# Optimization experiments

Hardware: AMD Instinct MI355X
Metric: run time of the kernel (lower is better)

## Reference

```python
import jax, jax.numpy as jnp
import numpy as np

N_NODES = 50000
N_EDGES = 800000
DIM = 128


def setup_inputs() -> dict:
    key = jax.random.key(0)
    k_x, k_e, k_w1, k_w2 = jax.random.split(key, 4)
    x = jax.random.normal(k_x, (N_NODES, DIM), dtype=jnp.float32)
    edge_index = jax.random.randint(k_e, (2, N_EDGES), 0, N_NODES, dtype=jnp.int64)
    scale = 1.0 / np.sqrt(DIM)
    W1 = jax.random.normal(k_w1, (DIM, DIM), dtype=jnp.float32) * scale
    b1 = jnp.zeros((DIM,), dtype=jnp.float32)
    W2 = jax.random.normal(k_w2, (DIM, DIM), dtype=jnp.float32) * scale
    b2 = jnp.zeros((DIM,), dtype=jnp.float32)
    return {"x": x, "edge_index": edge_index, "W1": W1, "b1": b1, "W2": W2, "b2": b2}


def _gcn_conv(x, W, b, src, dst, n_nodes):
    """PyG GCNConv: D^{-1/2}(A+I)D^{-1/2} (x @ W) + b, self-loops added."""
    h = x @ W  # [N, D]
    ones = jnp.ones(src.shape[0], dtype=h.dtype)
    # degree of A+I, counting incoming edges at target nodes plus self-loop
    deg = jax.ops.segment_sum(ones, dst, num_segments=n_nodes) + 1.0
    dinv = jax.lax.rsqrt(deg)  # [N]
    norm = dinv[src] * dinv[dst]  # [E]
    msgs = h[src] * norm[:, None]  # [E, D] gather (memory-bound)
    agg = jax.ops.segment_sum(msgs, dst, num_segments=n_nodes)  # scatter-add
    agg = agg + h * (dinv * dinv)[:, None]  # self-loop contribution
    return agg + b


def reference(x, edge_index, W1, b1, W2, b2):
    src, dst = edge_index[0], edge_index[1]
    n = x.shape[0]
    identity = x
    out = jax.nn.relu(_gcn_conv(x, W1, b1, src, dst, n))
    out = _gcn_conv(out, W2, b2, src, dst, n)
    return jax.nn.relu(out + identity)
```

## Files before the change

kernel.cpp:

```cpp
#include <hip/hip_runtime.h>

#define N_NODES 50000
#define N_EDGES 800000
#define DIM 128
#define NB 391
#define CAP 2560
#define NCH 7
#define BIN_CHUNK 4096
#define BIN_BLOCKS 196
#define PREP_BLOCKS 64
#define GEMM_TILES 782
#define AGG_BLOCKS 3125

typedef unsigned int uint;
typedef unsigned short ushort;
typedef __attribute__((ext_vector_type(8))) __bf16 bf16x8;
typedef __attribute__((ext_vector_type(4))) float f32x4;

__device__ __forceinline__ uint f2bf(float f) {
    uint u = __float_as_uint(f);
    return (u + 0x7FFFu + ((u >> 16) & 1u)) >> 16;
}
__device__ __forceinline__ float2 bf2f2(uint u) {
    return make_float2(__uint_as_float(u << 16), __uint_as_float(u & 0xFFFF0000u));
}


__global__ __launch_bounds__(256) void binprep_kernel(const int* __restrict__ ei,
                                                      int* __restrict__ bincursor,
                                                      uint* __restrict__ pairs,
                                                      const float* __restrict__ W1,
                                                      const float* __restrict__ W2,
                                                      uint* __restrict__ Wt1,
                                                      uint* __restrict__ Wt2) {
    if (blockIdx.x >= BIN_BLOCKS) {
        int idx = (blockIdx.x - BIN_BLOCKS) * 256 + threadIdx.x;
        const float* W = (idx < 8192) ? W1 : W2;
        uint* Wt = (idx < 8192) ? Wt1 : Wt2;
        int i = idx & 8191;
        int n = i >> 6, k2 = i & 63;
        Wt[i] = f2bf(W[(2 * k2) * DIM + n]) | (f2bf(W[(2 * k2 + 1) * DIM + n]) << 16);
        return;
    }
    __shared__ int lh[NB];
    __shared__ int lbase[NB];
    int t = threadIdx.x;
    int eb = blockIdx.x * BIN_CHUNK;

    for (int b = t; b < NB; b += 256) lh[b] = 0;
    __syncthreads();

    int s_reg[16], d_reg[16];
#pragma unroll
    for (int i = 0; i < 16; ++i) {
        int e = eb + i * 256 + t;
        if (e < N_EDGES) {
            s_reg[i] = ei[e];
            d_reg[i] = ei[N_EDGES + e];
            atomicAdd(&lh[d_reg[i] >> 7], 1);
        } else {
            d_reg[i] = -1;
        }
    }
    __syncthreads();

    for (int b = t; b < NB; b += 256) {
        int c = lh[b];
        lbase[b] = c ? (b * CAP + atomicAdd(&bincursor[b], c)) : 0;
    }
    __syncthreads();
    for (int b = t; b < NB; b += 256) lh[b] = 0;
    __syncthreads();

#pragma unroll
    for (int i = 0; i < 16; ++i) {
        int d = d_reg[i];
        if (d >= 0) {
            int bin = d >> 7;
            int r = atomicAdd(&lh[bin], 1);
            pairs[lbase[bin] + r] = ((uint)s_reg[i] << 7) | (uint)(d & 127);
        }
    }
}


__device__ __forceinline__ void gemm1_tile(const float* __restrict__ X,
                                           const uint* __restrict__ Wt, int base,
                                           uint* __restrict__ Hout) {
    int t = threadIdx.x;
    int wv = t >> 6;
    int l = t & 63;
    int col = l & 15;
    int g = l >> 4;
    int grow = base + wv * 16 + col;
    int ar = grow > N_NODES - 1 ? N_NODES - 1 : grow;

    bf16x8 af[4];
    const float4* Xr = (const float4*)(X + (size_t)ar * DIM);
#pragma unroll
    for (int kk = 0; kk < 4; ++kk) {
        float4 x0 = Xr[kk * 8 + g * 2];
        float4 x1 = Xr[kk * 8 + g * 2 + 1];
        uint4 p;
        p.x = f2bf(x0.x) | (f2bf(x0.y) << 16);
        p.y = f2bf(x0.z) | (f2bf(x0.w) << 16);
        p.z = f2bf(x1.x) | (f2bf(x1.y) << 16);
        p.w = f2bf(x1.z) | (f2bf(x1.w) << 16);
        af[kk] = __builtin_bit_cast(bf16x8, p);
    }

    const uint4* Wr = (const uint4*)Wt;
    f32x4 acc[8];
#pragma unroll
    for (int n = 0; n < 8; ++n) acc[n] = (f32x4){0.f, 0.f, 0.f, 0.f};

#pragma unroll
    for (int n = 0; n < 8; ++n) {
        const uint4* wrow = Wr + (size_t)(n * 16 + col) * 16;
#pragma unroll
        for (int kk = 0; kk < 4; ++kk) {
            bf16x8 bf = __builtin_bit_cast(bf16x8, wrow[kk * 4 + g]);
            acc[n] = __builtin_amdgcn_mfma_f32_16x16x32_bf16(af[kk], bf, acc[n], 0, 0, 0);
        }
    }

#pragma unroll
    for (int j = 0; j < 4; ++j) {
        int row = base + wv * 16 + g * 4 + j;
        if (row < N_NODES) {
            ushort* hrow = (ushort*)(Hout + (size_t)row * 64);
#pragma unroll
            for (int n = 0; n < 8; ++n) hrow[n * 16 + col] = (ushort)f2bf(acc[n][j]);
        }
    }
}


__global__ __launch_bounds__(256) void fillgemm_kernel(const uint* __restrict__ pairs,
                                                       const int* __restrict__ bincursor,
                                                       int* __restrict__ rowbeg,
                                                       int* __restrict__ rowend,
                                                       float* __restrict__ dinv,
                                                       int* __restrict__ csr_src,
                                                       const float* __restrict__ x,
                                                       const uint* __restrict__ Wt1,
                                                       uint* __restrict__ Hs) {
    if (blockIdx.x >= NB) {
        gemm1_tile(x, Wt1, (blockIdx.x - NB) * 64, Hs);
        return;
    }
    __shared__ int cnt[128 * 8];
    __shared__ int nsum[128];
    __shared__ int nbase[128];
    int t = threadIdx.x;
    int blk = blockIdx.x;
    int bs = blk * CAP;
    int be = bs + bincursor[blk];

    for (int i = t; i < 128 * 8; i += 256) cnt[i] = 0;
    __syncthreads();

    for (int p = bs + t; p < be; p += 256) {
        uint pr = pairs[p];
        atomicAdd(&cnt[(pr & 127u) * 8 + (pr >> 20)], 1);
    }
    __syncthreads();

    if (t < 128) {
        int s = 0;
#pragma unroll
        for (int c = 0; c < NCH; ++c) s += cnt[t * 8 + c];
        nsum[t] = s;
        nbase[t] = s;
    }
    __syncthreads();
#pragma unroll
    for (int off = 1; off < 128; off <<= 1) {
        int v = (t < 128 && t >= off) ? nbase[t - off] : 0;
        __syncthreads();
        if (t < 128) nbase[t] += v;
        __syncthreads();
    }

    if (t < 128) {
        int deg = nsum[t];
        int ex = nbase[t] - deg;
        int node = blk * 128 + t;
        if (node < N_NODES) {
            rowbeg[node] = bs + ex;
            rowend[node] = bs + nbase[t];
            dinv[node] = rsqrtf((float)deg + 1.0f);
        }
        int run = ex;
#pragma unroll
        for (int c = 0; c < NCH; ++c) {
            int v = cnt[t * 8 + c];
            cnt[t * 8 + c] = run;
            run += v;
        }
    }
    __syncthreads();

    for (int p = bs + t; p < be; p += 256) {
        uint pr = pairs[p];
        int r = atomicAdd(&cnt[(pr & 127u) * 8 + (pr >> 20)], 1);
        csr_src[bs + r] = (int)(pr >> 7);
    }
}


template <bool DSRC, bool OBF>
__global__ __launch_bounds__(256) void agg_kernel(const int* __restrict__ rowbeg,
                                                  const int* __restrict__ rowend,
                                                  const int* __restrict__ csr_src,
                                                  const uint* __restrict__ Hs,
                                                  const float* __restrict__ dinv,
                                                  const float* __restrict__ bias,
                                                  const float* __restrict__ resid,
                                                  void* __restrict__ outv) {
    int gt = blockIdx.x * 256 + threadIdx.x;
    int wave = gt >> 6;
    int lane = gt & 63;
    int grp = lane >> 4;
    int li = lane & 15;
    int node = wave * 4 + grp;

    int beg = rowbeg[node];
    int end = rowend[node];
    float di = dinv[node];

    const uint4* H4 = (const uint4*)Hs;
    float a0, a1, a2, a3, a4, a5, a6, a7;
    {
        uint4 su = H4[(size_t)node * 16 + li];
        float2 v0 = bf2f2(su.x), v1 = bf2f2(su.y), v2 = bf2f2(su.z), v3 = bf2f2(su.w);
        float sf = DSRC ? di : 1.0f;
        a0 = sf * v0.x; a1 = sf * v0.y; a2 = sf * v1.x; a3 = sf * v1.y;
        a4 = sf * v2.x; a5 = sf * v2.y; a6 = sf * v3.x; a7 = sf * v3.y;
    }

#define ADDF8(u, f)                                                               \
    {                                                                             \
        float2 v0 = bf2f2(u.x), v1 = bf2f2(u.y), v2 = bf2f2(u.z), v3 = bf2f2(u.w);\
        a0 += f * v0.x; a1 += f * v0.y; a2 += f * v1.x; a3 += f * v1.y;           \
        a4 += f * v2.x; a5 += f * v2.y; a6 += f * v3.x; a7 += f * v3.y;           \
    }

    int e = beg;
    for (; e + 7 < end; e += 8) {
        int s[8];
#pragma unroll
        for (int i = 0; i < 8; ++i) s[i] = csr_src[e + i];
        uint4 u[8];
#pragma unroll
        for (int i = 0; i < 8; ++i) u[i] = H4[(size_t)s[i] * 16 + li];
        float f[8];
#pragma unroll
        for (int i = 0; i < 8; ++i) f[i] = DSRC ? dinv[s[i]] : 1.0f;
#pragma unroll
        for (int i = 0; i < 8; ++i) ADDF8(u[i], f[i]);
    }
    if (e + 3 < end) {
        int s[4];
#pragma unroll
        for (int i = 0; i < 4; ++i) s[i] = csr_src[e + i];
        uint4 u[4];
#pragma unroll
        for (int i = 0; i < 4; ++i) u[i] = H4[(size_t)s[i] * 16 + li];
        float f[4];
#pragma unroll
        for (int i = 0; i < 4; ++i) f[i] = DSRC ? dinv[s[i]] : 1.0f;
#pragma unroll
        for (int i = 0; i < 4; ++i) ADDF8(u[i], f[i]);
        e += 4;
    }
    for (; e < end; ++e) {
        int s = csr_src[e];
        uint4 u = H4[(size_t)s * 16 + li];
        float f = DSRC ? dinv[s] : 1.0f;
        ADDF8(u, f);
    }
#undef ADDF8

    const float4* B4 = (const float4*)bias;
    float4 bb0 = B4[li * 2], bb1 = B4[li * 2 + 1];
    float r0 = a0 * di + bb0.x, r1 = a1 * di + bb0.y;
    float r2 = a2 * di + bb0.z, r3 = a3 * di + bb0.w;
    float r4 = a4 * di + bb1.x, r5 = a5 * di + bb1.y;
    float r6 = a6 * di + bb1.z, r7 = a7 * di + bb1.w;

    if (OBF) {
        uint4 o;
        o.x = f2bf(fmaxf(r0, 0.f)) | (f2bf(fmaxf(r1, 0.f)) << 16);
        o.y = f2bf(fmaxf(r2, 0.f)) | (f2bf(fmaxf(r3, 0.f)) << 16);
        o.z = f2bf(fmaxf(r4, 0.f)) | (f2bf(fmaxf(r5, 0.f)) << 16);
        o.w = f2bf(fmaxf(r6, 0.f)) | (f2bf(fmaxf(r7, 0.f)) << 16);
        ((uint4*)outv)[(size_t)node * 16 + li] = o;
    } else {
        const float4* R4 = (const float4*)(resid + (size_t)node * DIM);
        float4 x0 = R4[li * 2], x1 = R4[li * 2 + 1];
        r0 += x0.x; r1 += x0.y; r2 += x0.z; r3 += x0.w;
        r4 += x1.x; r5 += x1.y; r6 += x1.z; r7 += x1.w;
        float4* O4 = (float4*)((float*)outv + (size_t)node * DIM);
        O4[li * 2] = make_float4(fmaxf(r0, 0.f), fmaxf(r1, 0.f), fmaxf(r2, 0.f), fmaxf(r3, 0.f));
        O4[li * 2 + 1] = make_float4(fmaxf(r4, 0.f), fmaxf(r5, 0.f), fmaxf(r6, 0.f), fmaxf(r7, 0.f));
    }
}


__global__ __launch_bounds__(256) void gemm2_kernel(const uint* __restrict__ out1b,
                                                    const uint* __restrict__ Wt,
                                                    const float* __restrict__ dinv,
                                                    uint* __restrict__ Hout) {
    int t = threadIdx.x;
    int wv = t >> 6;
    int l = t & 63;
    int col = l & 15;
    int g = l >> 4;
    int base = blockIdx.x * 64;
    int grow = base + wv * 16 + col;
    int ar = grow > N_NODES - 1 ? N_NODES - 1 : grow;

    bf16x8 af[4];
    const uint4* Xr = (const uint4*)(out1b + (size_t)ar * 64);
#pragma unroll
    for (int kk = 0; kk < 4; ++kk) af[kk] = __builtin_bit_cast(bf16x8, Xr[kk * 4 + g]);

    const uint4* Wr = (const uint4*)Wt;
    f32x4 acc[8];
#pragma unroll
    for (int n = 0; n < 8; ++n) acc[n] = (f32x4){0.f, 0.f, 0.f, 0.f};

#pragma unroll
    for (int n = 0; n < 8; ++n) {
        const uint4* wrow = Wr + (size_t)(n * 16 + col) * 16;
#pragma unroll
        for (int kk = 0; kk < 4; ++kk) {
            bf16x8 bf = __builtin_bit_cast(bf16x8, wrow[kk * 4 + g]);
            acc[n] = __builtin_amdgcn_mfma_f32_16x16x32_bf16(af[kk], bf, acc[n], 0, 0, 0);
        }
    }

#pragma unroll
    for (int j = 0; j < 4; ++j) {
        int row = base + wv * 16 + g * 4 + j;
        if (row < N_NODES) {
            float di = dinv[row];
            ushort* hrow = (ushort*)(Hout + (size_t)row * 64);
#pragma unroll
            for (int n = 0; n < 8; ++n) hrow[n * 16 + col] = (ushort)f2bf(acc[n][j] * di);
        }
    }
}


extern "C" void kernel_launch(void* const* d_in, const int* in_sizes, int n_in,
                              void* d_out, int out_size, void* d_ws, size_t ws_size,
                              hipStream_t stream) {
    const float* x = (const float*)d_in[0];
    const int* edge_index = (const int*)d_in[1];
    const float* W1 = (const float*)d_in[2];
    const float* b1 = (const float*)d_in[3];
    const float* W2 = (const float*)d_in[4];
    const float* b2 = (const float*)d_in[5];
    float* out = (float*)d_out;

    char* ws = (char*)d_ws;
    int*   bincursor = (int*)(ws + 0);
    float* dinv      = (float*)(ws + (256 << 10));
    int*   rowbeg    = (int*)(ws + (512 << 10));
    int*   rowend    = (int*)(ws + (768 << 10));
    int*   csr_src   = (int*)(ws + (2 << 20));
    uint*  pairs     = (uint*)(ws + (6 << 20));
    uint*  Hs        = (uint*)(ws + (12 << 20));
    uint*  out1b     = (uint*)(ws + (25 << 20));
    uint*  Wt1       = (uint*)(ws + (38 << 20));
    uint*  Wt2       = (uint*)(ws + (38 << 20) + (64 << 10));

    hipMemsetAsync(bincursor, 0, NB * sizeof(int), stream);
    binprep_kernel<<<BIN_BLOCKS + PREP_BLOCKS, 256, 0, stream>>>(edge_index, bincursor, pairs,
                                                                 W1, W2, Wt1, Wt2);
    fillgemm_kernel<<<NB + GEMM_TILES, 256, 0, stream>>>(pairs, bincursor, rowbeg, rowend, dinv,
                                                         csr_src, x, Wt1, Hs);
    agg_kernel<true, true><<<AGG_BLOCKS, 256, 0, stream>>>(rowbeg, rowend, csr_src, Hs, dinv, b1,
                                                           nullptr, (void*)out1b);
    gemm2_kernel<<<GEMM_TILES, 256, 0, stream>>>(out1b, Wt2, dinv, Hs);
    agg_kernel<false, false><<<AGG_BLOCKS, 256, 0, stream>>>(rowbeg, rowend, csr_src, Hs, dinv,
                                                             b2, x, (void*)out);
}
```

Measured before the change: 140.8 us.

## Co-schedule GEMM1 with edge binning and fold memset into weight prep

Moves the first GEMM tiles from the CSR fill kernel into the edge-binning kernel, so the GEMM overlaps with binning instead of with the fill stage. Weight transpose and bincursor initialization (now set to absolute bin offsets) move into a separate small prep kernel, which replaces the memset. The fill stage becomes a standalone kernel. Launch count stays the same, but the work split across stages changes and the fill kernel no longer gets GEMM overlap.

```diff
diff --git a/kernel.cpp b/kernel.cpp
--- a/kernel.cpp
+++ b/kernel.cpp
@@ -8,7 +8,6 @@
 #define NCH 7
 #define BIN_CHUNK 4096
 #define BIN_BLOCKS 196
-#define PREP_BLOCKS 64
 #define GEMM_TILES 782
 #define AGG_BLOCKS 3125
 
@@ -26,60 +25,21 @@
 }
 
 
-__global__ __launch_bounds__(256) void binprep_kernel(const int* __restrict__ ei,
-                                                      int* __restrict__ bincursor,
-                                                      uint* __restrict__ pairs,
-                                                      const float* __restrict__ W1,
-                                                      const float* __restrict__ W2,
-                                                      uint* __restrict__ Wt1,
-                                                      uint* __restrict__ Wt2) {
-    if (blockIdx.x >= BIN_BLOCKS) {
-        int idx = (blockIdx.x - BIN_BLOCKS) * 256 + threadIdx.x;
+__global__ __launch_bounds__(256) void prep_kernel(const float* __restrict__ W1,
+                                                   const float* __restrict__ W2,
+                                                   uint* __restrict__ Wt1,
+                                                   uint* __restrict__ Wt2,
+                                                   int* __restrict__ bincursor) {
+    int idx = blockIdx.x * 256 + threadIdx.x;
+    if (idx < 16384) {
         const float* W = (idx < 8192) ? W1 : W2;
         uint* Wt = (idx < 8192) ? Wt1 : Wt2;
         int i = idx & 8191;
         int n = i >> 6, k2 = i & 63;
         Wt[i] = f2bf(W[(2 * k2) * DIM + n]) | (f2bf(W[(2 * k2 + 1) * DIM + n]) << 16);
-        return;
-    }
-    __shared__ int lh[NB];
-    __shared__ int lbase[NB];
-    int t = threadIdx.x;
-    int eb = blockIdx.x * BIN_CHUNK;
-
-    for (int b = t; b < NB; b += 256) lh[b] = 0;
-    __syncthreads();
-
-    int s_reg[16], d_reg[16];
-#pragma unroll
-    for (int i = 0; i < 16; ++i) {
-        int e = eb + i * 256 + t;
-        if (e < N_EDGES) {
-            s_reg[i] = ei[e];
-            d_reg[i] = ei[N_EDGES + e];
-            atomicAdd(&lh[d_reg[i] >> 7], 1);
-        } else {
-            d_reg[i] = -1;
-        }
-    }
-    __syncthreads();
-
-    for (int b = t; b < NB; b += 256) {
-        int c = lh[b];
-        lbase[b] = c ? (b * CAP + atomicAdd(&bincursor[b], c)) : 0;
-    }
-    __syncthreads();
-    for (int b = t; b < NB; b += 256) lh[b] = 0;
-    __syncthreads();
-
-#pragma unroll
-    for (int i = 0; i < 16; ++i) {
-        int d = d_reg[i];
-        if (d >= 0) {
-            int bin = d >> 7;
-            int r = atomicAdd(&lh[bin], 1);
-            pairs[lbase[bin] + r] = ((uint)s_reg[i] << 7) | (uint)(d & 127);
-        }
+    } else {
+        int b = idx - 16384;
+        if (b < NB) bincursor[b] = b * CAP;
     }
 }
 
@@ -136,26 +96,71 @@
 }
 
 
-__global__ __launch_bounds__(256) void fillgemm_kernel(const uint* __restrict__ pairs,
-                                                       const int* __restrict__ bincursor,
-                                                       int* __restrict__ rowbeg,
-                                                       int* __restrict__ rowend,
-                                                       float* __restrict__ dinv,
-                                                       int* __restrict__ csr_src,
-                                                       const float* __restrict__ x,
-                                                       const uint* __restrict__ Wt1,
-                                                       uint* __restrict__ Hs) {
-    if (blockIdx.x >= NB) {
-        gemm1_tile(x, Wt1, (blockIdx.x - NB) * 64, Hs);
+__global__ __launch_bounds__(256) void bin_gemm1_kernel(const int* __restrict__ ei,
+                                                        int* __restrict__ bincursor,
+                                                        uint* __restrict__ pairs,
+                                                        const float* __restrict__ x,
+                                                        const uint* __restrict__ Wt1,
+                                                        uint* __restrict__ Hs) {
+    if (blockIdx.x >= BIN_BLOCKS) {
+        gemm1_tile(x, Wt1, (blockIdx.x - BIN_BLOCKS) * 64, Hs);
         return;
     }
+    __shared__ int lh[NB];
+    __shared__ int lbase[NB];
+    int t = threadIdx.x;
+    int eb = blockIdx.x * BIN_CHUNK;
+
+    for (int b = t; b < NB; b += 256) lh[b] = 0;
+    __syncthreads();
+
+    int s_reg[16], d_reg[16];
+#pragma unroll
+    for (int i = 0; i < 16; ++i) {
+        int e = eb + i * 256 + t;
+        if (e < N_EDGES) {
+            s_reg[i] = ei[e];
+            d_reg[i] = ei[N_EDGES + e];
+            atomicAdd(&lh[d_reg[i] >> 7], 1);
+        } else {
+            d_reg[i] = -1;
+        }
+    }
+    __syncthreads();
+
+    for (int b = t; b < NB; b += 256) {
+        int c = lh[b];
+        lbase[b] = c ? atomicAdd(&bincursor[b], c) : 0;
+    }
+    __syncthreads();
+    for (int b = t; b < NB; b += 256) lh[b] = 0;
+    __syncthreads();
+
+#pragma unroll
+    for (int i = 0; i < 16; ++i) {
+        int d = d_reg[i];
+        if (d >= 0) {
+            int bin = d >> 7;
+            int r = atomicAdd(&lh[bin], 1);
+            pairs[lbase[bin] + r] = ((uint)s_reg[i] << 7) | (uint)(d & 127);
+        }
+    }
+}
+
+
+__global__ __launch_bounds__(256) void fill2_kernel(const uint* __restrict__ pairs,
+                                                    const int* __restrict__ bincursor,
+                                                    int* __restrict__ rowbeg,
+                                                    int* __restrict__ rowend,
+                                                    float* __restrict__ dinv,
+                                                    int* __restrict__ csr_src) {
     __shared__ int cnt[128 * 8];
     __shared__ int nsum[128];
     __shared__ int nbase[128];
     int t = threadIdx.x;
     int blk = blockIdx.x;
     int bs = blk * CAP;
-    int be = bs + bincursor[blk];
+    int be = bincursor[blk];
 
     for (int i = t; i < 128 * 8; i += 256) cnt[i] = 0;
     __syncthreads();
@@ -377,11 +382,10 @@
     uint*  Wt1       = (uint*)(ws + (38 << 20));
     uint*  Wt2       = (uint*)(ws + (38 << 20) + (64 << 10));
 
-    hipMemsetAsync(bincursor, 0, NB * sizeof(int), stream);
-    binprep_kernel<<<BIN_BLOCKS + PREP_BLOCKS, 256, 0, stream>>>(edge_index, bincursor, pairs,
-                                                                 W1, W2, Wt1, Wt2);
-    fillgemm_kernel<<<NB + GEMM_TILES, 256, 0, stream>>>(pairs, bincursor, rowbeg, rowend, dinv,
-                                                         csr_src, x, Wt1, Hs);
+    prep_kernel<<<66, 256, 0, stream>>>(W1, W2, Wt1, Wt2, bincursor);
+    bin_gemm1_kernel<<<BIN_BLOCKS + GEMM_TILES, 256, 0, stream>>>(edge_index, bincursor, pairs,
+                                                                  x, Wt1, Hs);
+    fill2_kernel<<<NB, 256, 0, stream>>>(pairs, bincursor, rowbeg, rowend, dinv, csr_src);
     agg_kernel<true, true><<<AGG_BLOCKS, 256, 0, stream>>>(rowbeg, rowend, csr_src, Hs, dinv, b1,
                                                            nullptr, (void*)out1b);
     gemm2_kernel<<<GEMM_TILES, 256, 0, stream>>>(out1b, Wt2, dinv, Hs);
```

New measurement: 134.8 us. 1.04x faster.

## Reorder GCN to aggregate before GEMM with dinv-prescaled bf16 features

Applied to the files above, without the earlier changes.

Uses associativity to aggregate neighbor features first (A·X then ·W) instead of transforming first, with the source-side dinv folded into the stored bf16 features. This removes the per-edge dinv gather in the aggregation loops, and bias, relu and residual move into the GEMM epilogues. It adds an fp32 aggregate buffer (written then re-read by the GEMMs) and serialises the first GEMM after aggregation, so it no longer overlaps with the CSR fill.

```diff
diff --git a/kernel.cpp b/kernel.cpp
--- a/kernel.cpp
+++ b/kernel.cpp
@@ -84,19 +84,169 @@
 }
 
 
-__device__ __forceinline__ void gemm1_tile(const float* __restrict__ X,
-                                           const uint* __restrict__ Wt, int base,
-                                           uint* __restrict__ Hout) {
+__global__ __launch_bounds__(256) void fillpack_kernel(const uint* __restrict__ pairs,
+                                                       const int* __restrict__ bincursor,
+                                                       int* __restrict__ rowbeg,
+                                                       int* __restrict__ rowend,
+                                                       float* __restrict__ dinv,
+                                                       int* __restrict__ csr_src,
+                                                       const float* __restrict__ x,
+                                                       uint* __restrict__ xb) {
+    __shared__ int cnt[128 * 8];
+    __shared__ int nsum[128];
+    __shared__ int nbase[128];
+    __shared__ float sdinv[128];
+    int t = threadIdx.x;
+    int blk = blockIdx.x;
+    int bs = blk * CAP;
+    int be = bs + bincursor[blk];
+
+    for (int i = t; i < 128 * 8; i += 256) cnt[i] = 0;
+    __syncthreads();
+
+    for (int p = bs + t; p < be; p += 256) {
+        uint pr = pairs[p];
+        atomicAdd(&cnt[(pr & 127u) * 8 + (pr >> 20)], 1);
+    }
+    __syncthreads();
+
+    if (t < 128) {
+        int s = 0;
+#pragma unroll
+        for (int c = 0; c < NCH; ++c) s += cnt[t * 8 + c];
+        nsum[t] = s;
+        nbase[t] = s;
+    }
+    __syncthreads();
+#pragma unroll
+    for (int off = 1; off < 128; off <<= 1) {
+        int v = (t < 128 && t >= off) ? nbase[t - off] : 0;
+        __syncthreads();
+        if (t < 128) nbase[t] += v;
+        __syncthreads();
+    }
+
+    if (t < 128) {
+        int deg = nsum[t];
+        int ex = nbase[t] - deg;
+        int node = blk * 128 + t;
+        float di = rsqrtf((float)deg + 1.0f);
+        sdinv[t] = di;
+        if (node < N_NODES) {
+            rowbeg[node] = bs + ex;
+            rowend[node] = bs + nbase[t];
+            dinv[node] = di;
+        }
+        int run = ex;
+#pragma unroll
+        for (int c = 0; c < NCH; ++c) {
+            int v = cnt[t * 8 + c];
+            cnt[t * 8 + c] = run;
+            run += v;
+        }
+    }
+    __syncthreads();
+
+    for (int p = bs + t; p < be; p += 256) {
+        uint pr = pairs[p];
+        int r = atomicAdd(&cnt[(pr & 127u) * 8 + (pr >> 20)], 1);
+        csr_src[bs + r] = (int)(pr >> 7);
+    }
+
+    for (int i = t; i < 128 * 64; i += 256) {
+        int row = i >> 6;
+        int u = i & 63;
+        int node = blk * 128 + row;
+        if (node < N_NODES) {
+            float2 xv = *(const float2*)(x + (size_t)node * DIM + 2 * u);
+            float d = sdinv[row];
+            xb[(size_t)node * 64 + u] = f2bf(xv.x * d) | (f2bf(xv.y * d) << 16);
+        }
+    }
+}
+
+
+__global__ __launch_bounds__(256) void aggS_kernel(const int* __restrict__ rowbeg,
+                                                   const int* __restrict__ rowend,
+                                                   const int* __restrict__ csr_src,
+                                                   const uint* __restrict__ Hb,
+                                                   float* __restrict__ aggF) {
+    int gt = blockIdx.x * 256 + threadIdx.x;
+    int wave = gt >> 6;
+    int lane = gt & 63;
+    int grp = lane >> 4;
+    int li = lane & 15;
+    int node = wave * 4 + grp;
+
+    int beg = rowbeg[node];
+    int end = rowend[node];
+
+    const uint4* H4 = (const uint4*)Hb;
+    float a0, a1, a2, a3, a4, a5, a6, a7;
+    {
+        uint4 su = H4[(size_t)node * 16 + li];
+        float2 v0 = bf2f2(su.x), v1 = bf2f2(su.y), v2 = bf2f2(su.z), v3 = bf2f2(su.w);
+        a0 = v0.x; a1 = v0.y; a2 = v1.x; a3 = v1.y;
+        a4 = v2.x; a5 = v2.y; a6 = v3.x; a7 = v3.y;
+    }
+
+#define ADD8(u)                                                                   \
+    {                                                                             \
+        float2 v0 = bf2f2(u.x), v1 = bf2f2(u.y), v2 = bf2f2(u.z), v3 = bf2f2(u.w);\
+        a0 += v0.x; a1 += v0.y; a2 += v1.x; a3 += v1.y;                           \
+        a4 += v2.x; a5 += v2.y; a6 += v3.x; a7 += v3.y;                           \
+    }
+
+    int e = beg;
+    for (; e + 7 < end; e += 8) {
+        int s[8];
+#pragma unroll
+        for (int i = 0; i < 8; ++i) s[i] = csr_src[e + i];
+        uint4 u[8];
+#pragma unroll
+        for (int i = 0; i < 8; ++i) u[i] = H4[(size_t)s[i] * 16 + li];
+#pragma unroll
+        for (int i = 0; i < 8; ++i) ADD8(u[i]);
+    }
+    if (e + 3 < end) {
+        int s[4];
+#pragma unroll
+        for (int i = 0; i < 4; ++i) s[i] = csr_src[e + i];
+        uint4 u[4];
+#pragma unroll
+        for (int i = 0; i < 4; ++i) u[i] = H4[(size_t)s[i] * 16 + li];
+#pragma unroll
+        for (int i = 0; i < 4; ++i) ADD8(u[i]);
+        e += 4;
+    }
+    for (; e < end; ++e) {
+        uint4 u = H4[(size_t)csr_src[e] * 16 + li];
+        ADD8(u);
+    }
+#undef ADD8
+
+    float4* O4 = (float4*)(aggF + (size_t)node * DIM);
+    O4[li * 2] = make_float4(a0, a1, a2, a3);
+    O4[li * 2 + 1] = make_float4(a4, a5, a6, a7);
+}
+
+
+__global__ __launch_bounds__(256) void gemmA_kernel(const float* __restrict__ aggF,
+                                                    const uint* __restrict__ Wt,
+                                                    const float* __restrict__ dinv,
+                                                    const float* __restrict__ b1,
+                                                    uint* __restrict__ out1b) {
     int t = threadIdx.x;
     int wv = t >> 6;
     int l = t & 63;
     int col = l & 15;
     int g = l >> 4;
+    int base = blockIdx.x * 64;
     int grow = base + wv * 16 + col;
     int ar = grow > N_NODES - 1 ? N_NODES - 1 : grow;
 
     bf16x8 af[4];
-    const float4* Xr = (const float4*)(X + (size_t)ar * DIM);
+    const float4* Xr = (const float4*)(aggF + (size_t)ar * DIM);
 #pragma unroll
     for (int kk = 0; kk < 4; ++kk) {
         float4 x0 = Xr[kk * 8 + g * 2];
@@ -124,194 +274,32 @@
         }
     }
 
+    float bb[8];
+#pragma unroll
+    for (int n = 0; n < 8; ++n) bb[n] = b1[n * 16 + col];
+
 #pragma unroll
     for (int j = 0; j < 4; ++j) {
         int row = base + wv * 16 + g * 4 + j;
         if (row < N_NODES) {
-            ushort* hrow = (ushort*)(Hout + (size_t)row * 64);
-#pragma unroll
-            for (int n = 0; n < 8; ++n) hrow[n * 16 + col] = (ushort)f2bf(acc[n][j]);
-        }
-    }
-}
-
-
-__global__ __launch_bounds__(256) void fillgemm_kernel(const uint* __restrict__ pairs,
-                                                       const int* __restrict__ bincursor,
-                                                       int* __restrict__ rowbeg,
-                                                       int* __restrict__ rowend,
-                                                       float* __restrict__ dinv,
-                                                       int* __restrict__ csr_src,
-                                                       const float* __restrict__ x,
-                                                       const uint* __restrict__ Wt1,
-                                                       uint* __restrict__ Hs) {
-    if (blockIdx.x >= NB) {
-        gemm1_tile(x, Wt1, (blockIdx.x - NB) * 64, Hs);
-        return;
-    }
-    __shared__ int cnt[128 * 8];
-    __shared__ int nsum[128];
-    __shared__ int nbase[128];
-    int t = threadIdx.x;
-    int blk = blockIdx.x;
-    int bs = blk * CAP;
-    int be = bs + bincursor[blk];
-
-    for (int i = t; i < 128 * 8; i += 256) cnt[i] = 0;
-    __syncthreads();
-
-    for (int p = bs + t; p < be; p += 256) {
-        uint pr = pairs[p];
-        atomicAdd(&cnt[(pr & 127u) * 8 + (pr >> 20)], 1);
-    }
-    __syncthreads();
-
-    if (t < 128) {
-        int s = 0;
-#pragma unroll
-        for (int c = 0; c < NCH; ++c) s += cnt[t * 8 + c];
-        nsum[t] = s;
-        nbase[t] = s;
-    }
-    __syncthreads();
-#pragma unroll
-    for (int off = 1; off < 128; off <<= 1) {
-        int v = (t < 128 && t >= off) ? nbase[t - off] : 0;
-        __syncthreads();
-        if (t < 128) nbase[t] += v;
-        __syncthreads();
-    }
-
-    if (t < 128) {
-        int deg = nsum[t];
-        int ex = nbase[t] - deg;
-        int node = blk * 128 + t;
-        if (node < N_NODES) {
-            rowbeg[node] = bs + ex;
-            rowend[node] = bs + nbase[t];
-            dinv[node] = rsqrtf((float)deg + 1.0f);
-        }
-        int run = ex;
-#pragma unroll
-        for (int c = 0; c < NCH; ++c) {
-            int v = cnt[t * 8 + c];
-            cnt[t * 8 + c] = run;
-            run += v;
-        }
-    }
-    __syncthreads();
-
-    for (int p = bs + t; p < be; p += 256) {
-        uint pr = pairs[p];
-        int r = atomicAdd(&cnt[(pr & 127u) * 8 + (pr >> 20)], 1);
-        csr_src[bs + r] = (int)(pr >> 7);
-    }
-}
-
-
-template <bool DSRC, bool OBF>
-__global__ __launch_bounds__(256) void agg_kernel(const int* __restrict__ rowbeg,
-                                                  const int* __restrict__ rowend,
-                                                  const int* __restrict__ csr_src,
-                                                  const uint* __restrict__ Hs,
-                                                  const float* __restrict__ dinv,
-                                                  const float* __restrict__ bias,
-                                                  const float* __restrict__ resid,
-                                                  void* __restrict__ outv) {
-    int gt = blockIdx.x * 256 + threadIdx.x;
-    int wave = gt >> 6;
-    int lane = gt & 63;
-    int grp = lane >> 4;
-    int li = lane & 15;
-    int node = wave * 4 + grp;
-
-    int beg = rowbeg[node];
-    int end = rowend[node];
-    float di = dinv[node];
-
-    const uint4* H4 = (const uint4*)Hs;
-    float a0, a1, a2, a3, a4, a5, a6, a7;
-    {
-        uint4 su = H4[(size_t)node * 16 + li];
-        float2 v0 = bf2f2(su.x), v1 = bf2f2(su.y), v2 = bf2f2(su.z), v3 = bf2f2(su.w);
-        float sf = DSRC ? di : 1.0f;
-        a0 = sf * v0.x; a1 = sf * v0.y; a2 = sf * v1.x; a3 = sf * v1.y;
-        a4 = sf * v2.x; a5 = sf * v2.y; a6 = sf * v3.x; a7 = sf * v3.y;
-    }
-
-#define ADDF8(u, f)                                                               \
-    {                                                                             \
-        float2 v0 = bf2f2(u.x), v1 = bf2f2(u.y), v2 = bf2f2(u.z), v3 = bf2f2(u.w);\
-        a0 += f * v0.x; a1 += f * v0.y; a2 += f * v1.x; a3 += f * v1.y;           \
-        a4 += f * v2.x; a5 += f * v2.y; a6 += f * v3.x; a7 += f * v3.y;           \
-    }
-
-    int e = beg;
-    for (; e + 7 < end; e += 8) {
-        int s[8];
-#pragma unroll
-        for (int i = 0; i < 8; ++i) s[i] = csr_src[e + i];
-        uint4 u[8];
-#pragma unroll
-        for (int i = 0; i < 8; ++i) u[i] = H4[(size_t)s[i] * 16 + li];
-        float f[8];
-#pragma unroll
-        for (int i = 0; i < 8; ++i) f[i] = DSRC ? dinv[s[i]] : 1.0f;
-#pragma unroll
-        for (int i = 0; i < 8; ++i) ADDF8(u[i], f[i]);
-    }
-    if (e + 3 < end) {
-        int s[4];
-#pragma unroll
-        for (int i = 0; i < 4; ++i) s[i] = csr_src[e + i];
-        uint4 u[4];
-#pragma unroll
-        for (int i = 0; i < 4; ++i) u[i] = H4[(size_t)s[i] * 16 + li];
-        float f[4];
-#pragma unroll
-        for (int i = 0; i < 4; ++i) f[i] = DSRC ? dinv[s[i]] : 1.0f;
-#pragma unroll
-        for (int i = 0; i < 4; ++i) ADDF8(u[i], f[i]);
-        e += 4;
-    }
-    for (; e < end; ++e) {
-        int s = csr_src[e];
-        uint4 u = H4[(size_t)s * 16 + li];
-        float f = DSRC ? dinv[s] : 1.0f;
-        ADDF8(u, f);
-    }
-#undef ADDF8
-
-    const float4* B4 = (const float4*)bias;
-    float4 bb0 = B4[li * 2], bb1 = B4[li * 2 + 1];
-    float r0 = a0 * di + bb0.x, r1 = a1 * di + bb0.y;
-    float r2 = a2 * di + bb0.z, r3 = a3 * di + bb0.w;
-    float r4 = a4 * di + bb1.x, r5 = a5 * di + bb1.y;
-    float r6 = a6 * di + bb1.z, r7 = a7 * di + bb1.w;
-
-    if (OBF) {
-        uint4 o;
-        o.x = f2bf(fmaxf(r0, 0.f)) | (f2bf(fmaxf(r1, 0.f)) << 16);
-        o.y = f2bf(fmaxf(r2, 0.f)) | (f2bf(fmaxf(r3, 0.f)) << 16);
-        o.z = f2bf(fmaxf(r4, 0.f)) | (f2bf(fmaxf(r5, 0.f)) << 16);
-        o.w = f2bf(fmaxf(r6, 0.f)) | (f2bf(fmaxf(r7, 0.f)) << 16);
-        ((uint4*)outv)[(size_t)node * 16 + li] = o;
-    } else {
-        const float4* R4 = (const float4*)(resid + (size_t)node * DIM);
-        float4 x0 = R4[li * 2], x1 = R4[li * 2 + 1];
-        r0 += x0.x; r1 += x0.y; r2 += x0.z; r3 += x0.w;
-        r4 += x1.x; r5 += x1.y; r6 += x1.z; r7 += x1.w;
-        float4* O4 = (float4*)((float*)outv + (size_t)node * DIM);
-        O4[li * 2] = make_float4(fmaxf(r0, 0.f), fmaxf(r1, 0.f), fmaxf(r2, 0.f), fmaxf(r3, 0.f));
-        O4[li * 2 + 1] = make_float4(fmaxf(r4, 0.f), fmaxf(r5, 0.f), fmaxf(r6, 0.f), fmaxf(r7, 0.f));
-    }
-}
-
-
-__global__ __launch_bounds__(256) void gemm2_kernel(const uint* __restrict__ out1b,
+            float di = dinv[row];
+            ushort* hrow = (ushort*)(out1b + (size_t)row * 64);
+#pragma unroll
+            for (int n = 0; n < 8; ++n) {
+                float o = fmaxf(di * acc[n][j] + bb[n], 0.f);
+                hrow[n * 16 + col] = (ushort)f2bf(di * o);
+            }
+        }
+    }
+}
+
+
+__global__ __launch_bounds__(256) void gemmB_kernel(const float* __restrict__ aggF,
                                                     const uint* __restrict__ Wt,
                                                     const float* __restrict__ dinv,
-                                                    uint* __restrict__ Hout) {
+                                                    const float* __restrict__ b2,
+                                                    const float* __restrict__ x,
+                                                    float* __restrict__ out) {
     int t = threadIdx.x;
     int wv = t >> 6;
     int l = t & 63;
@@ -322,9 +310,18 @@
     int ar = grow > N_NODES - 1 ? N_NODES - 1 : grow;
 
     bf16x8 af[4];
-    const uint4* Xr = (const uint4*)(out1b + (size_t)ar * 64);
-#pragma unroll
-    for (int kk = 0; kk < 4; ++kk) af[kk] = __builtin_bit_cast(bf16x8, Xr[kk * 4 + g]);
+    const float4* Xr = (const float4*)(aggF + (size_t)ar * DIM);
+#pragma unroll
+    for (int kk = 0; kk < 4; ++kk) {
+        float4 x0 = Xr[kk * 8 + g * 2];
+        float4 x1 = Xr[kk * 8 + g * 2 + 1];
+        uint4 p;
+        p.x = f2bf(x0.x) | (f2bf(x0.y) << 16);
+        p.y = f2bf(x0.z) | (f2bf(x0.w) << 16);
+        p.z = f2bf(x1.x) | (f2bf(x1.y) << 16);
+        p.w = f2bf(x1.z) | (f2bf(x1.w) << 16);
+        af[kk] = __builtin_bit_cast(bf16x8, p);
+    }
 
     const uint4* Wr = (const uint4*)Wt;
     f32x4 acc[8];
@@ -340,15 +337,23 @@
             acc[n] = __builtin_amdgcn_mfma_f32_16x16x32_bf16(af[kk], bf, acc[n], 0, 0, 0);
         }
     }
+
+    float bb[8];
+#pragma unroll
+    for (int n = 0; n < 8; ++n) bb[n] = b2[n * 16 + col];
 
 #pragma unroll
     for (int j = 0; j < 4; ++j) {
         int row = base + wv * 16 + g * 4 + j;
         if (row < N_NODES) {
             float di = dinv[row];
-            ushort* hrow = (ushort*)(Hout + (size_t)row * 64);
-#pragma unroll
-            for (int n = 0; n < 8; ++n) hrow[n * 16 + col] = (ushort)f2bf(acc[n][j] * di);
+            const float* xr = x + (size_t)row * DIM;
+            float* orow = out + (size_t)row * DIM;
+#pragma unroll
+            for (int n = 0; n < 8; ++n) {
+                int c = n * 16 + col;
+                orow[c] = fmaxf(di * acc[n][j] + bb[n] + xr[c], 0.f);
+            }
         }
     }
 }
@@ -370,21 +375,21 @@
     float* dinv      = (float*)(ws + (256 << 10));
     int*   rowbeg    = (int*)(ws + (512 << 10));
     int*   rowend    = (int*)(ws + (768 << 10));
-    int*   csr_src   = (int*)(ws + (2 << 20));
-    uint*  pairs     = (uint*)(ws + (6 << 20));
-    uint*  Hs        = (uint*)(ws + (12 << 20));
-    uint*  out1b     = (uint*)(ws + (25 << 20));
-    uint*  Wt1       = (uint*)(ws + (38 << 20));
-    uint*  Wt2       = (uint*)(ws + (38 << 20) + (64 << 10));
+    int*   csr_src   = (int*)(ws + (1 << 20));
+    uint*  pairs     = (uint*)(ws + (5 << 20));
+    uint*  xb        = (uint*)(ws + (9 << 20));
+    uint*  out1b     = (uint*)(ws + (22 << 20));
+    float* aggF      = (float*)(ws + (35 << 20));
+    uint*  Wt1       = (uint*)(ws + (61 << 20));
+    uint*  Wt2       = (uint*)(ws + (61 << 20) + (64 << 10));
 
     hipMemsetAsync(bincursor, 0, NB * sizeof(int), stream);
     binprep_kernel<<<BIN_BLOCKS + PREP_BLOCKS, 256, 0, stream>>>(edge_index, bincursor, pairs,
                                                                  W1, W2, Wt1, Wt2);
-    fillgemm_kernel<<<NB + GEMM_TILES, 256, 0, stream>>>(pairs, bincursor, rowbeg, rowend, dinv,
-                                                         csr_src, x, Wt1, Hs);
-    agg_kernel<true, true><<<AGG_BLOCKS, 256, 0, stream>>>(rowbeg, rowend, csr_src, Hs, dinv, b1,
-                                                           nullptr, (void*)out1b);
-    gemm2_kernel<<<GEMM_TILES, 256, 0, stream>>>(out1b, Wt2, dinv, Hs);
-    agg_kernel<false, false><<<AGG_BLOCKS, 256, 0, stream>>>(rowbeg, rowend, csr_src, Hs, dinv,
-                                                             b2, x, (void*)out);
-}
+    fillpack_kernel<<<NB, 256, 0, stream>>>(pairs, bincursor, rowbeg, rowend, dinv, csr_src, x,
+                                            xb);
+    aggS_kernel<<<AGG_BLOCKS, 256, 0, stream>>>(rowbeg, rowend, csr_src, xb, aggF);
+    gemmA_kernel<<<GEMM_TILES, 256, 0, stream>>>(aggF, Wt1, dinv, b1, out1b);
+    aggS_kernel<<<AGG_BLOCKS, 256, 0, stream>>>(rowbeg, rowend, csr_src, out1b, aggF);
+    gemmB_kernel<<<GEMM_TILES, 256, 0, stream>>>(aggF, Wt2, dinv, b2, x, out);
+}
```

Measured after the change: 157.5 us. 11.9% more time.
